# Optimization experiments

Hardware: AMD Instinct MI355X
Metric: run time of the kernel (lower is better)

## Reference

```python
import jax, jax.numpy as jnp
import numpy as np

NUM_OPS = 8
D = 1024
B = 8192


def setup_inputs() -> dict:
    key = jax.random.key(0)
    k1, k2, k3, k4 = jax.random.split(key, 4)
    x = jax.random.normal(k1, (B, D), dtype=jnp.float32)
    logits = 0.001 * jax.random.normal(k2, (NUM_OPS,), dtype=jnp.float32)
    Ws = jax.random.normal(k3, (NUM_OPS, D, D), dtype=jnp.float32) * (1.0 / np.sqrt(D))
    bs = jax.random.normal(k4, (NUM_OPS, D), dtype=jnp.float32) * 0.01
    return {"x": x, "logits": logits, "Ws": Ws, "bs": bs, "num_on_samples": 2}


def reference(x, logits, Ws, bs, num_on_samples):
    # non_stochastic_call: top-k op selection by architecture logits,
    # dispatch x to the selected ops, sum-combine the results.
    _, top_k_ids = jax.lax.top_k(logits, num_on_samples)  # [k]
    W_sel = jnp.take(Ws, top_k_ids, axis=0)  # [k, D, D]
    b_sel = jnp.take(bs, top_k_ids, axis=0)  # [k, D]
    # each op is Dense(D->D) + relu: [k, B, D]
    op_results = jax.nn.relu(jnp.einsum('bd,kde->kbe', x, W_sel) + b_sel[:, None, :])
    return jnp.sum(op_results, axis=0)  # [B, D]
```

## Files before the change

### kernel.cpp

```cpp
#include <hip/hip_runtime.h>
#include <hip/hip_bf16.h>

#define NUM_OPS 8
#define D 1024
#define B_ROWS 8192

typedef unsigned short ushort_t;
typedef __attribute__((ext_vector_type(8))) short bf16x8;
typedef __attribute__((ext_vector_type(4))) float f32x4;
typedef __attribute__((ext_vector_type(4))) float float4v;
typedef __attribute__((ext_vector_type(8))) unsigned short ushort8;

__device__ __forceinline__ unsigned short f2bf(float f) {
    union { float f; unsigned int u; } v; v.f = f;
    unsigned int u = v.u;
    unsigned int lsb = (u >> 16) & 1u;
    u += 0x7fffu + lsb;
    return (unsigned short)(u >> 16);
}

__device__ __forceinline__ void load_lds16(const void* g, void* l) {
    __builtin_amdgcn_global_load_lds(
        (const __attribute__((address_space(1))) void*)g,
        (__attribute__((address_space(3))) void*)l,
        16, 0, 0);
}

__device__ __forceinline__ void top2(const float* __restrict__ logits, int& i0, int& i1) {
    float best = -__builtin_inff(); i0 = 0;
    for (int i = 0; i < NUM_OPS; ++i) { float v = logits[i]; if (v > best) { best = v; i0 = i; } }
    float best2 = -__builtin_inff(); i1 = 0;
    for (int i = 0; i < NUM_OPS; ++i) {
        if (i == i0) continue;
        float v = logits[i]; if (v > best2) { best2 = v; i1 = i; }
    }
}

__global__ void convert_x(const float* __restrict__ x, ushort_t* __restrict__ xb) {
    int i = (blockIdx.x * 256 + threadIdx.x) * 8;
    float4v v0 = *(const float4v*)(x + i);
    float4v v1 = *(const float4v*)(x + i + 4);
    ushort8 o;
    o[0] = f2bf(v0[0]); o[1] = f2bf(v0[1]); o[2] = f2bf(v0[2]); o[3] = f2bf(v0[3]);
    o[4] = f2bf(v1[0]); o[5] = f2bf(v1[1]); o[6] = f2bf(v1[2]); o[7] = f2bf(v1[3]);
    *(ushort8*)(xb + i) = o;
}

__global__ void gather_frag_W(const float* __restrict__ Ws,
                              const float* __restrict__ logits,
                              ushort_t* __restrict__ Wf) {
    __shared__ float t[32][33];
    int s0, s1; top2(logits, s0, s1);
    const int b  = blockIdx.x;
    const int nt = b & 31, kt = (b >> 5) & 31, e = b >> 10;
    const int td = kt * 32, te = nt * 32;
    const int tx = threadIdx.x & 31, ty = threadIdx.x >> 5;
    const float* W = Ws + (size_t)(e ? s1 : s0) * D * D;
    #pragma unroll
    for (int r = 0; r < 4; ++r)
        t[ty + 8 * r][tx] = W[(size_t)(td + ty + 8 * r) * D + te + tx];
    __syncthreads();
    const int vid = threadIdx.x;
    if (vid < 128) {
        const int n_l = vid & 31, kg = vid >> 5;
        const int n = te + n_l, k0 = td + kg * 8;
        const int u = k0 >> 6, kk = (k0 >> 5) & 1, lq = (k0 >> 3) & 3;
        const int P = n >> 6, c4 = (n >> 4) & 3, l15 = n & 15;
        const int lane = lq * 16 + l15;
        const int fi = ((e * 16 + P) * 16 + u) * 8 + c4 * 2 + kk;
        ushort8 o;
        #pragma unroll
        for (int j = 0; j < 8; ++j) o[j] = f2bf(t[kg * 8 + j][n_l]);
        *(ushort8*)(Wf + (size_t)fi * 512 + lane * 8) = o;
    }
}

__device__ __forceinline__ void stageA(const ushort_t* __restrict__ xbf, int brow,
                                       int u, ushort_t* dst, int tid) {
    #pragma unroll
    for (int q = 0; q < 4; ++q) {
        const int c   = q * 256 + tid;
        const int rr  = c >> 3;
        const int gcb = ((c & 7) * 16) ^ ((rr & 7) << 4);
        load_lds16(xbf + (size_t)(brow + rr) * D + u * 64 + (gcb >> 1), dst + c * 8);
    }
}

#define SB()    __builtin_amdgcn_sched_barrier(0)
#define PRIO1() __builtin_amdgcn_s_setprio(1)
#define PRIO0() __builtin_amdgcn_s_setprio(0)
#define VM(N)   do { asm volatile("s_waitcnt vmcnt(" #N ")" ::: "memory"); } while (0)

#define RD_A(CA)                                                                   \
    do {                                                                           \
        _Pragma("unroll") for (int kk = 0; kk < 2; ++kk)                           \
        _Pragma("unroll") for (int m = 0; m < 4; ++m)                              \
            a[kk][m] = *(const bf16x8*)((const char*)(CA) +                        \
                (size_t)((wr * 64 + m * 16 + l15) * 128) + (kk ? x1 : x0));        \
    } while (0)

#define LD_B(SET, E, U)                                                            \
    do {                                                                           \
        const ushort_t* cb = Wf + ((size_t)(((E) * 16 + P) * 16 + (U)) * 8) * 512  \
                              + lane * 8;                                          \
        _Pragma("unroll") for (int i = 0; i < 8; ++i)                              \
            SET[i] = *(const bf16x8*)(cb + (size_t)i * 512);                       \
    } while (0)

#define MM(E, SET)                                                                 \
    do {                                                                           \
        PRIO1();                                                                   \
        _Pragma("unroll") for (int kk = 0; kk < 2; ++kk)                           \
        _Pragma("unroll") for (int m = 0; m < 4; ++m)                              \
        _Pragma("unroll") for (int c4 = 0; c4 < 4; ++c4)                           \
            acc[E][m][c4] = __builtin_amdgcn_mfma_f32_16x16x32_bf16(               \
                a[kk][m], SET[c4 * 2 + kk], acc[E][m][c4], 0, 0, 0);               \
        PRIO0();                                                                   \
    } while (0)

#define TILE(CA, DA, SU, U, VMN, DOSTG, DOBAR)                                     \
    do {                                                                           \
        RD_A(CA);                                                                  \
        LD_B(bY, 1, (U));                                                          \
        if (DOSTG) stageA(xbf, brow, (SU), DA, tid);                               \
        SB();                                                                      \
        MM(0, bX);                                                                 \
        if ((U) < 15) LD_B(bX, 0, (U) + 1);                                        \
        SB();                                                                      \
        MM(1, bY);                                                                 \
        VM(VMN);                                                                   \
        if (DOBAR) __builtin_amdgcn_s_barrier();                                   \
    } while (0)

__global__ __launch_bounds__(256, 2)
void gemm_dual(const ushort_t* __restrict__ xbf, const ushort_t* __restrict__ Wf,
               const float* __restrict__ bs, const float* __restrict__ logits,
               float* __restrict__ out) {
    __shared__ __align__(16) ushort_t As0[128 * 64], As1[128 * 64], As2[128 * 64];

    const int tid  = threadIdx.x;
    const int wv   = tid >> 6;
    const int lane = tid & 63;
    const int wr   = wv >> 1, wc = wv & 1;
    const int l15  = lane & 15, lq = lane >> 4;
    const int swz  = (l15 & 7) << 4;
    const int x0   = (lq * 16) ^ swz;
    const int x1   = (64 + lq * 16) ^ swz;

    const int bid  = blockIdx.x;
    const int brow = (bid & 63) * 128;
    const int P    = (bid >> 6) * 2 + wc;

    f32x4  acc[2][4][4] = {};
    bf16x8 a[2][4];
    bf16x8 bX[8], bY[8];

    stageA(xbf, brow, 0, As0, tid);
    stageA(xbf, brow, 1, As1, tid);
    LD_B(bX, 0, 0);
    SB();
    VM(12);
    __builtin_amdgcn_s_barrier();

    TILE(As0, As2,  2,  0, 12, true,  true);
    TILE(As1, As0,  3,  1, 12, true,  true);
    TILE(As2, As1,  4,  2, 12, true,  true);
    TILE(As0, As2,  5,  3, 12, true,  true);
    TILE(As1, As0,  6,  4, 12, true,  true);
    TILE(As2, As1,  7,  5, 12, true,  true);
    TILE(As0, As2,  8,  6, 12, true,  true);
    TILE(As1, As0,  9,  7, 12, true,  true);
    TILE(As2, As1, 10,  8, 12, true,  true);
    TILE(As0, As2, 11,  9, 12, true,  true);
    TILE(As1, As0, 12, 10, 12, true,  true);
    TILE(As2, As1, 13, 11, 12, true,  true);
    TILE(As0, As2, 14, 12, 12, true,  true);
    TILE(As1, As0, 15, 13, 12, true,  true);
    TILE(As2, As1,  0, 14,  8, false, true);
    TILE(As0, As1,  0, 15,  0, false, false);

    int s0, s1; top2(logits, s0, s1);
    #pragma unroll
    for (int c4 = 0; c4 < 4; ++c4) {
        const int col = P * 64 + c4 * 16 + l15;
        const float b0 = bs[s0 * D + col];
        const float b1 = bs[s1 * D + col];
        #pragma unroll
        for (int m = 0; m < 4; ++m) {
            const int rbase = brow + wr * 64 + m * 16 + lq * 4;
            #pragma unroll
            for (int i = 0; i < 4; ++i) {
                float v0 = acc[0][m][c4][i] + b0; v0 = v0 > 0.f ? v0 : 0.f;
                float v1 = acc[1][m][c4][i] + b1; v1 = v1 > 0.f ? v1 : 0.f;
                out[(size_t)(rbase + i) * D + col] = v0 + v1;
            }
        }
    }
}

extern "C" void kernel_launch(void* const* d_in, const int* in_sizes, int n_in,
                              void* d_out, int out_size, void* d_ws, size_t ws_size,
                              hipStream_t stream) {
    const float* x      = (const float*)d_in[0];
    const float* logits = (const float*)d_in[1];
    const float* Ws     = (const float*)d_in[2];
    const float* bs     = (const float*)d_in[3];
    float* out = (float*)d_out;

    char* ws = (char*)d_ws;
    ushort_t* xbf = (ushort_t*)ws;
    ushort_t* Wf  = (ushort_t*)(ws + (size_t)B_ROWS * D * 2);

    convert_x<<<(B_ROWS * D) / (256 * 8), 256, 0, stream>>>(x, xbf);
    gather_frag_W<<<2 * 32 * 32, 256, 0, stream>>>(Ws, logits, Wf);

    gemm_dual<<<512, 256, 0, stream>>>(xbf, Wf, bs, logits, out);
}
```

Before: 53.34 us.

## Switch to double-buffered A staging with per-tile B loads and new Wf layout

Changes the packed weight layout to 32-column granules and restructures the main GEMM loop. It now uses two LDS buffers instead of a triple-buffer ring and loads both experts' B fragments inside each tile, dropping the ping-pong register sets and the sched_barrier interleaving. Block-to-tile mapping changes from column-major (bid&63 rows) to row-major with 8 column tiles per row. This simplifies scheduling and may reduce register pressure, at the risk of exposing global B-load latency that was previously prefetched a tile ahead.

```diff
diff --git a/kernel.cpp b/kernel.cpp
--- a/kernel.cpp
+++ b/kernel.cpp
@@ -65,9 +65,9 @@
         const int n_l = vid & 31, kg = vid >> 5;
         const int n = te + n_l, k0 = td + kg * 8;
         const int u = k0 >> 6, kk = (k0 >> 5) & 1, lq = (k0 >> 3) & 3;
-        const int P = n >> 6, c4 = (n >> 4) & 3, l15 = n & 15;
+        const int p = n >> 5, n16 = (n >> 4) & 1, l15 = n & 15;
         const int lane = lq * 16 + l15;
-        const int fi = ((e * 16 + P) * 16 + u) * 8 + c4 * 2 + kk;
+        const int fi = (((e * 32 + p) * 16 + u) * 2 + kk) * 2 + n16;
         ushort8 o;
         #pragma unroll
         for (int j = 0; j < 8; ++j) o[j] = f2bf(t[kg * 8 + j][n_l]);
@@ -75,60 +75,50 @@
     }
 }
 
-__device__ __forceinline__ void stageA(const ushort_t* __restrict__ xbf, int brow,
-                                       int u, ushort_t* dst, int tid) {
-    #pragma unroll
-    for (int q = 0; q < 4; ++q) {
-        const int c   = q * 256 + tid;
+__device__ __forceinline__ void stageA128(const ushort_t* __restrict__ xbf,
+                                          int brow, int u, ushort_t* dst,
+                                          int tid, int wv) {
+    #pragma unroll
+    for (int it = 0; it < 4; ++it) {
+        const int c   = it * 256 + tid;
         const int rr  = c >> 3;
-        const int gcb = ((c & 7) * 16) ^ ((rr & 7) << 4);
-        load_lds16(xbf + (size_t)(brow + rr) * D + u * 64 + (gcb >> 1), dst + c * 8);
-    }
-}
-
-#define SB()    __builtin_amdgcn_sched_barrier(0)
+        const int cb  = (c & 7) * 16;
+        const int gcb = cb ^ ((rr & 7) << 4);
+        const ushort_t* g = xbf + (size_t)(brow + rr) * D + u * 64 + (gcb >> 1);
+        ushort_t* l = dst + (it * 256 + wv * 64) * 8;
+        load_lds16(g, l);
+    }
+}
+
 #define PRIO1() __builtin_amdgcn_s_setprio(1)
 #define PRIO0() __builtin_amdgcn_s_setprio(0)
-#define VM(N)   do { asm volatile("s_waitcnt vmcnt(" #N ")" ::: "memory"); } while (0)
-
-#define RD_A(CA)                                                                   \
+
+#define TILE(CUR, NXT, U, STG, VN, DOBAR)                                          \
     do {                                                                           \
+        if (STG) stageA128(xbf, brow, (U) + 1, NXT, tid, wv);                      \
+        bf16x8 b[2][2][2][2];                                                      \
+        _Pragma("unroll") for (int e = 0; e < 2; ++e)                              \
+        _Pragma("unroll") for (int pp = 0; pp < 2; ++pp)                           \
+        _Pragma("unroll") for (int kk = 0; kk < 2; ++kk)                           \
+        _Pragma("unroll") for (int n16 = 0; n16 < 2; ++n16) {                      \
+            const int fi = (((e * 32 + p0 + pp) * 16 + (U)) * 2 + kk) * 2 + n16;   \
+            b[e][pp][kk][n16] = *(const bf16x8*)(Wf + (size_t)fi * 512 + lane * 8);\
+        }                                                                          \
+        bf16x8 a[2][4];                                                            \
         _Pragma("unroll") for (int kk = 0; kk < 2; ++kk)                           \
         _Pragma("unroll") for (int m = 0; m < 4; ++m)                              \
-            a[kk][m] = *(const bf16x8*)((const char*)(CA) +                        \
+            a[kk][m] = *(const bf16x8*)((const char*)(CUR) +                       \
                 (size_t)((wr * 64 + m * 16 + l15) * 128) + (kk ? x1 : x0));        \
-    } while (0)
-
-#define LD_B(SET, E, U)                                                            \
-    do {                                                                           \
-        const ushort_t* cb = Wf + ((size_t)(((E) * 16 + P) * 16 + (U)) * 8) * 512  \
-                              + lane * 8;                                          \
-        _Pragma("unroll") for (int i = 0; i < 8; ++i)                              \
-            SET[i] = *(const bf16x8*)(cb + (size_t)i * 512);                       \
-    } while (0)
-
-#define MM(E, SET)                                                                 \
-    do {                                                                           \
         PRIO1();                                                                   \
         _Pragma("unroll") for (int kk = 0; kk < 2; ++kk)                           \
+        _Pragma("unroll") for (int e = 0; e < 2; ++e)                              \
         _Pragma("unroll") for (int m = 0; m < 4; ++m)                              \
-        _Pragma("unroll") for (int c4 = 0; c4 < 4; ++c4)                           \
-            acc[E][m][c4] = __builtin_amdgcn_mfma_f32_16x16x32_bf16(               \
-                a[kk][m], SET[c4 * 2 + kk], acc[E][m][c4], 0, 0, 0);               \
+        _Pragma("unroll") for (int pp = 0; pp < 2; ++pp)                           \
+        _Pragma("unroll") for (int n16 = 0; n16 < 2; ++n16)                        \
+            acc[e][m][pp][n16] = __builtin_amdgcn_mfma_f32_16x16x32_bf16(          \
+                a[kk][m], b[e][pp][kk][n16], acc[e][m][pp][n16], 0, 0, 0);         \
         PRIO0();                                                                   \
-    } while (0)
-
-#define TILE(CA, DA, SU, U, VMN, DOSTG, DOBAR)                                     \
-    do {                                                                           \
-        RD_A(CA);                                                                  \
-        LD_B(bY, 1, (U));                                                          \
-        if (DOSTG) stageA(xbf, brow, (SU), DA, tid);                               \
-        SB();                                                                      \
-        MM(0, bX);                                                                 \
-        if ((U) < 15) LD_B(bX, 0, (U) + 1);                                        \
-        SB();                                                                      \
-        MM(1, bY);                                                                 \
-        VM(VMN);                                                                   \
+        asm volatile("s_waitcnt vmcnt(" #VN ")" ::: "memory");                     \
         if (DOBAR) __builtin_amdgcn_s_barrier();                                   \
     } while (0)
 
@@ -136,7 +126,7 @@
 void gemm_dual(const ushort_t* __restrict__ xbf, const ushort_t* __restrict__ Wf,
                const float* __restrict__ bs, const float* __restrict__ logits,
                float* __restrict__ out) {
-    __shared__ __align__(16) ushort_t As0[128 * 64], As1[128 * 64], As2[128 * 64];
+    __shared__ __align__(16) ushort_t As0[128 * 64], As1[128 * 64];
 
     const int tid  = threadIdx.x;
     const int wv   = tid >> 6;
@@ -148,50 +138,48 @@
     const int x1   = (64 + lq * 16) ^ swz;
 
     const int bid  = blockIdx.x;
-    const int brow = (bid & 63) * 128;
-    const int P    = (bid >> 6) * 2 + wc;
-
-    f32x4  acc[2][4][4] = {};
-    bf16x8 a[2][4];
-    bf16x8 bX[8], bY[8];
-
-    stageA(xbf, brow, 0, As0, tid);
-    stageA(xbf, brow, 1, As1, tid);
-    LD_B(bX, 0, 0);
-    SB();
-    VM(12);
+    const int brow = (bid >> 3) * 128;
+    const int bcol = (bid & 7) * 128;
+    const int p0   = (bcol >> 5) + wc * 2;
+
+    f32x4 acc[2][4][2][2] = {};
+
+    stageA128(xbf, brow, 0, As0, tid, wv);
+    asm volatile("s_waitcnt vmcnt(0)" ::: "memory");
     __builtin_amdgcn_s_barrier();
 
-    TILE(As0, As2,  2,  0, 12, true,  true);
-    TILE(As1, As0,  3,  1, 12, true,  true);
-    TILE(As2, As1,  4,  2, 12, true,  true);
-    TILE(As0, As2,  5,  3, 12, true,  true);
-    TILE(As1, As0,  6,  4, 12, true,  true);
-    TILE(As2, As1,  7,  5, 12, true,  true);
-    TILE(As0, As2,  8,  6, 12, true,  true);
-    TILE(As1, As0,  9,  7, 12, true,  true);
-    TILE(As2, As1, 10,  8, 12, true,  true);
-    TILE(As0, As2, 11,  9, 12, true,  true);
-    TILE(As1, As0, 12, 10, 12, true,  true);
-    TILE(As2, As1, 13, 11, 12, true,  true);
-    TILE(As0, As2, 14, 12, 12, true,  true);
-    TILE(As1, As0, 15, 13, 12, true,  true);
-    TILE(As2, As1,  0, 14,  8, false, true);
-    TILE(As0, As1,  0, 15,  0, false, false);
-
-    int s0, s1; top2(logits, s0, s1);
-    #pragma unroll
-    for (int c4 = 0; c4 < 4; ++c4) {
-        const int col = P * 64 + c4 * 16 + l15;
-        const float b0 = bs[s0 * D + col];
-        const float b1 = bs[s1 * D + col];
+    TILE(As0, As1,  0, true, 12, true);
+    TILE(As1, As0,  1, true, 12, true);
+    TILE(As0, As1,  2, true, 12, true);
+    TILE(As1, As0,  3, true, 12, true);
+    TILE(As0, As1,  4, true, 12, true);
+    TILE(As1, As0,  5, true, 12, true);
+    TILE(As0, As1,  6, true, 12, true);
+    TILE(As1, As0,  7, true, 12, true);
+    TILE(As0, As1,  8, true, 12, true);
+    TILE(As1, As0,  9, true, 12, true);
+    TILE(As0, As1, 10, true, 12, true);
+    TILE(As1, As0, 11, true, 12, true);
+    TILE(As0, As1, 12, true, 12, true);
+    TILE(As1, As0, 13, true, 12, true);
+    TILE(As0, As1, 14, true, 12, true);
+    TILE(As1, As0, 15, false, 0, false);
+
+    int i0, i1; top2(logits, i0, i1);
+    #pragma unroll
+    for (int pp = 0; pp < 2; ++pp)
+    #pragma unroll
+    for (int n16 = 0; n16 < 2; ++n16) {
+        const int col = bcol + wc * 64 + pp * 32 + n16 * 16 + l15;
+        const float b0 = bs[i0 * D + col];
+        const float b1 = bs[i1 * D + col];
         #pragma unroll
         for (int m = 0; m < 4; ++m) {
             const int rbase = brow + wr * 64 + m * 16 + lq * 4;
             #pragma unroll
             for (int i = 0; i < 4; ++i) {
-                float v0 = acc[0][m][c4][i] + b0; v0 = v0 > 0.f ? v0 : 0.f;
-                float v1 = acc[1][m][c4][i] + b1; v1 = v1 > 0.f ? v1 : 0.f;
+                float v0 = acc[0][m][pp][n16][i] + b0; v0 = v0 > 0.f ? v0 : 0.f;
+                float v1 = acc[1][m][pp][n16][i] + b1; v1 = v1 > 0.f ? v1 : 0.f;
                 out[(size_t)(rbase + i) * D + col] = v0 + v1;
             }
         }
```

Result: faster. 52.02 us (-2.5%).
